# Kernel tuning notes

Measured on AMD Instinct MI355X. Metric: run time of the kernel, lower is better.

## Reference

```python
import jax, jax.numpy as jnp
import numpy as np

L_PAIRS = 2
K_NEG = 64
TEMP = 0.1
EPS = 1e-8  # torch F.cosine_similarity default eps


def _cos(a, b):
    # cosine similarity along last axis, torch-style eps clamping of norms
    na = jnp.maximum(jnp.linalg.norm(a, axis=-1), EPS)
    nb = jnp.maximum(jnp.linalg.norm(b, axis=-1), EPS)
    return jnp.sum(a * b, axis=-1) / (na * nb)


def setup_inputs() -> dict:
    D, N, d = 64, 4096, 512
    key = jax.random.key(0)
    k0, k1, k2, k3 = jax.random.split(key, 4)
    return {
        "I_embeddings": jax.random.normal(k0, (D, N, d), dtype=jnp.float32),
        "g0": jax.random.normal(k1, (d,), dtype=jnp.float32),
        "g1": jax.random.normal(k2, (d,), dtype=jnp.float32),
        "g2": jax.random.normal(k3, (d,), dtype=jnp.float32),
    }


def reference(I_embeddings, g0, g1, g2):
    D, N, d = I_embeddings.shape
    T = TEMP

    # per-embedding full sum: [D, d]
    sums = jnp.sum(I_embeddings, axis=1)

    # hard-negative sums: drop the top-K rows by L2 norm per embedding
    norms = jnp.linalg.norm(I_embeddings, axis=2)              # [D, N]
    _, topk_idx = jax.lax.top_k(norms, K_NEG)                  # [D, K]
    keep = jnp.ones((D, N), dtype=bool)
    keep = keep.at[jnp.arange(D)[:, None], topk_idx].set(False)
    sums_neg = jnp.sum(I_embeddings * keep[:, :, None], axis=1)  # [D, d]

    samples = jnp.concatenate([sums, sums_neg], axis=0)        # [2D, d]

    # positive pairs (i, i+L)
    P = D - L_PAIRS
    i_idx = jnp.arange(P)
    j_idx = i_idx + L_PAIRS

    # candidates per pair: arange(2D) with i and j removed (i < j)
    base = jnp.arange(2 * D - 2)                               # [2D-2]
    cand = base[None, :] + (base[None, :] >= i_idx[:, None]).astype(base.dtype)
    cand = cand + (cand >= j_idx[:, None]).astype(cand.dtype)  # [P, 2D-2]

    # random choice of K_NEG negatives per pair (deterministic key)
    key = jax.random.key(42)
    keys = jax.random.split(key, P)
    perm = jax.vmap(lambda k: jax.random.permutation(k, 2 * D - 2))(keys)[:, :K_NEG]
    sel = jnp.take_along_axis(cand, perm, axis=1)              # [P, K]
    negs = samples[sel]                                        # [P, K, d]

    pos_ij = _cos(g1, jax.lax.stop_gradient(g2)) / T           # scalar
    pos_ji = _cos(g2, jax.lax.stop_gradient(g1)) / T           # scalar

    s_i = sums[i_idx]                                          # [P, d]
    s_j = sums[j_idx]
    sim_i = _cos(s_i[:, None, :], negs) / T                    # [P, K]
    sim_j = _cos(s_j[:, None, :], negs) / T

    # -log( exp(pos) / (exp(pos) + sum exp(sim)) ) = logaddexp(pos, lse(sim)) - pos
    loss_i = jnp.logaddexp(pos_ij, jax.nn.logsumexp(sim_i, axis=1)) - pos_ij  # [P]
    loss_j = jnp.logaddexp(pos_ji, jax.nn.logsumexp(sim_j, axis=1)) - pos_ji

    return jnp.sum(loss_i + loss_j)
```

## Files before the change

kernel.cpp:

```cpp
#include <hip/hip_runtime.h>
#include <stdint.h>

#define D_EMB   64
#define N_ROWS  4096
#define DIM     512
#define KNEG    64
#define P_PAIRS 62
#define BPE     32
#define ROWS_PER_BLK (N_ROWS / BPE)
#define EPSN    1e-8f
#define INV_T   10.0f

__device__ __forceinline__ uint32_t rotl32(uint32_t v, uint32_t r) {
  return (v << r) | (v >> (32u - r));
}

__device__ __forceinline__ void threefry(uint32_t k0, uint32_t k1,
                                         uint32_t c0, uint32_t c1,
                                         uint32_t& o0, uint32_t& o1) {
  uint32_t ks0 = k0, ks1 = k1, ks2 = k0 ^ k1 ^ 0x1BD11BDAu;
  uint32_t x0 = c0 + ks0, x1 = c1 + ks1;
#define RG(a,b,c,d) \
  x0 += x1; x1 = rotl32(x1,a); x1 ^= x0; \
  x0 += x1; x1 = rotl32(x1,b); x1 ^= x0; \
  x0 += x1; x1 = rotl32(x1,c); x1 ^= x0; \
  x0 += x1; x1 = rotl32(x1,d); x1 ^= x0;
  RG(13,15,26,6)   x0 += ks1; x1 += ks2 + 1u;
  RG(17,29,16,24)  x0 += ks2; x1 += ks0 + 2u;
  RG(13,15,26,6)   x0 += ks0; x1 += ks1 + 3u;
  RG(17,29,16,24)  x0 += ks1; x1 += ks2 + 4u;
  RG(13,15,26,6)   x0 += ks2; x1 += ks0 + 5u;
#undef RG
  o0 = x0; o1 = x1;
}

__global__ __launch_bounds__(256, 8) void k_pass1(const float* __restrict__ I,
                                                  float* __restrict__ partial,
                                                  float* __restrict__ norms) {
  const int e = blockIdx.x / BPE, b = blockIdx.x % BPE;
  const int t = threadIdx.x, lane = t & 63, w = t >> 6;
  const float4* base = reinterpret_cast<const float4*>(I) + (size_t)e * N_ROWS * (DIM / 4);
  float acc[8] = {0.f,0.f,0.f,0.f,0.f,0.f,0.f,0.f};
  __shared__ float lds[4 * DIM];
  __shared__ float nlds[ROWS_PER_BLK];
  const int nbase = b * ROWS_PER_BLK;
  for (int i = 0; i < ROWS_PER_BLK / 4; ++i) {
    const int n = nbase + i * 4 + w;
    const float4* row = base + (size_t)n * (DIM / 4);
    float4 A = row[lane];
    float4 B = row[lane + 64];
    acc[0] += A.x; acc[1] += A.y; acc[2] += A.z; acc[3] += A.w;
    acc[4] += B.x; acc[5] += B.y; acc[6] += B.z; acc[7] += B.w;
    float sq = A.x*A.x + A.y*A.y + A.z*A.z + A.w*A.w
             + B.x*B.x + B.y*B.y + B.z*B.z + B.w*B.w;
#pragma unroll
    for (int off = 32; off; off >>= 1) sq += __shfl_xor(sq, off);
    if (lane == 0) nlds[i * 4 + w] = sqrtf(sq);
  }
  const int p0 = 4 * lane;
#pragma unroll
  for (int q = 0; q < 4; ++q) {
    lds[w * DIM + p0 + q]       = acc[q];
    lds[w * DIM + 256 + p0 + q] = acc[4 + q];
  }
  __syncthreads();
  float s0 = lds[t] + lds[DIM + t] + lds[2*DIM + t] + lds[3*DIM + t];
  float s1 = lds[256 + t] + lds[DIM + 256 + t] + lds[2*DIM + 256 + t] + lds[3*DIM + 256 + t];
  float* out = partial + (size_t)(e * BPE + b) * DIM;
  out[t] = s0;
  out[256 + t] = s1;
  if (t < ROWS_PER_BLK) norms[e * N_ROWS + nbase + t] = nlds[t];
}

__global__ __launch_bounds__(512) void k_embed(const float* __restrict__ I,
                                               const float* __restrict__ partial,
                                               const float* __restrict__ norms,
                                               const float* __restrict__ g1,
                                               const float* __restrict__ g2,
                                               float* __restrict__ samples,
                                               float* __restrict__ snorm,
                                               float* __restrict__ posp) {
  const int e = blockIdx.x;
  const int t = threadIdx.x, lane = t & 63, w = t >> 6;
  __shared__ float rA[8], rB[8], rC[8];

  if (e == D_EMB) {
    float x = g1[t], y = g2[t];
    float d = x * y, sa = x * x, sb = y * y;
#pragma unroll
    for (int off = 32; off; off >>= 1) {
      d  += __shfl_xor(d, off);
      sa += __shfl_xor(sa, off);
      sb += __shfl_xor(sb, off);
    }
    if (lane == 0) { rA[w] = d; rB[w] = sa; rC[w] = sb; }
    __syncthreads();
    if (t == 0) {
      float dt = 0.f, s1 = 0.f, s2 = 0.f;
      for (int q = 0; q < 8; ++q) { dt += rA[q]; s1 += rB[q]; s2 += rC[q]; }
      posp[0] = dt / (fmaxf(sqrtf(s1), EPSN) * fmaxf(sqrtf(s2), EPSN)) * INV_T;
    }
    return;
  }

  float v[8];
#pragma unroll
  for (int q = 0; q < 8; ++q) v[q] = norms[e * N_ROWS + q * DIM + t];
  float lmax = v[0]; int lidx = t;
#pragma unroll
  for (int q = 1; q < 8; ++q)
    if (v[q] > lmax) { lmax = v[q]; lidx = q * DIM + t; }

  __shared__ float wbv[8];
  __shared__ int   wbi[8];
  __shared__ int   topidx[KNEG];
  for (int k = 0; k < KNEG; ++k) {
    float bv = lmax; int bi = lidx;
#pragma unroll
    for (int off = 32; off; off >>= 1) {
      float ov = __shfl_xor(bv, off);
      int   oi = __shfl_xor(bi, off);
      if (ov > bv || (ov == bv && oi < bi)) { bv = ov; bi = oi; }
    }
    if (lane == 0) { wbv[w] = bv; wbi[w] = bi; }
    __syncthreads();
    float fv = wbv[0]; int fi = wbi[0];
#pragma unroll
    for (int q = 1; q < 8; ++q)
      if (wbv[q] > fv || (wbv[q] == fv && wbi[q] < fi)) { fv = wbv[q]; fi = wbi[q]; }
    if (t == (fi & (DIM - 1))) {
      v[fi >> 9] = -1e30f;
      lmax = v[0]; lidx = t;
#pragma unroll
      for (int q = 1; q < 8; ++q)
        if (v[q] > lmax) { lmax = v[q]; lidx = q * DIM + t; }
    }
    if (t == 0) topidx[k] = fi;
    __syncthreads();
  }

  float s = 0.f;
  for (int b2 = 0; b2 < BPE; ++b2)
    s += partial[(size_t)(e * BPE + b2) * DIM + t];

  const float* base = I + (size_t)e * N_ROWS * DIM;
  float a = 0.f;
#pragma unroll 4
  for (int k = 0; k < KNEG; ++k)
    a += base[(size_t)topidx[k] * DIM + t];
  float sn = s - a;

  float q1 = s * s, q2 = sn * sn;
#pragma unroll
  for (int off = 32; off; off >>= 1) {
    q1 += __shfl_xor(q1, off);
    q2 += __shfl_xor(q2, off);
  }
  if (lane == 0) { rA[w] = q1; rB[w] = q2; }
  __syncthreads();
  if (t == 0) {
    float n1 = 0.f, n2 = 0.f;
    for (int q = 0; q < 8; ++q) { n1 += rA[q]; n2 += rB[q]; }
    snorm[e]         = fmaxf(sqrtf(n1), EPSN);
    snorm[D_EMB + e] = fmaxf(sqrtf(n2), EPSN);
  }
  samples[(size_t)e * DIM + t]           = s;
  samples[(size_t)(D_EMB + e) * DIM + t] = sn;
}

__global__ __launch_bounds__(256) void k_pair(const float* __restrict__ samples,
                                              const float* __restrict__ snorm,
                                              const float* __restrict__ posp,
                                              float* __restrict__ pairloss) {
  const int p = blockIdx.x;
  const int t = threadIdx.x, lane = t & 63, w = t >> 6;
  __shared__ uint32_t bits[126];
  __shared__ uint32_t sk[2];
  __shared__ int      sel[KNEG];
  __shared__ float    simi[KNEG], simj[KNEG];

  if (t == 0) {
    uint32_t kh, kl, a, b;
    threefry(0u, 42u, 0u, (uint32_t)p, kh, kl);
    threefry(kh, kl, 0u, 1u, a, b);
    sk[0] = a; sk[1] = b;
  }
  __syncthreads();
  if (t < 126) {
    uint32_t a, b;
    threefry(sk[0], sk[1], 0u, (uint32_t)t, a, b);
    bits[t] = a ^ b;
  }
  __syncthreads();
  if (t < 126) {
    const uint32_t myb = bits[t];
    int rank = 0;
    for (int j = 0; j < 126; ++j) {
      const uint32_t bj = bits[j];
      rank += ((bj < myb) || (bj == myb && j < t)) ? 1 : 0;
    }
    if (rank < KNEG) {
      int vv = t + (t >= p ? 1 : 0);
      vv += (vv >= p + 2 ? 1 : 0);
      sel[rank] = vv;
    }
  }
  __syncthreads();

  const float4* S = reinterpret_cast<const float4*>(samples);
  const float4 siA = S[p * 128 + lane],       siB = S[p * 128 + 64 + lane];
  const float4 sjA = S[(p + 2) * 128 + lane], sjB = S[(p + 2) * 128 + 64 + lane];
  const float ni = snorm[p], nj = snorm[p + 2];
  for (int k = w; k < KNEG; k += 4) {
    const int r = sel[k];
    const float4 vA = S[r * 128 + lane], vB = S[r * 128 + 64 + lane];
    float di = siA.x*vA.x + siA.y*vA.y + siA.z*vA.z + siA.w*vA.w
             + siB.x*vB.x + siB.y*vB.y + siB.z*vB.z + siB.w*vB.w;
    float dj = sjA.x*vA.x + sjA.y*vA.y + sjA.z*vA.z + sjA.w*vA.w
             + sjB.x*vB.x + sjB.y*vB.y + sjB.z*vB.z + sjB.w*vB.w;
#pragma unroll
    for (int off = 32; off; off >>= 1) {
      di += __shfl_xor(di, off);
      dj += __shfl_xor(dj, off);
    }
    if (lane == 0) {
      const float nr = snorm[r];
      simi[k] = di / (ni * nr) * INV_T;
      simj[k] = dj / (nj * nr) * INV_T;
    }
  }
  __syncthreads();
  if (t < KNEG) {
    const float xi = simi[t], xj = simj[t];
    float mi = xi, mj = xj;
#pragma unroll
    for (int off = 32; off; off >>= 1) {
      mi = fmaxf(mi, __shfl_xor(mi, off));
      mj = fmaxf(mj, __shfl_xor(mj, off));
    }
    float ei = expf(xi - mi), ej = expf(xj - mj);
#pragma unroll
    for (int off = 32; off; off >>= 1) {
      ei += __shfl_xor(ei, off);
      ej += __shfl_xor(ej, off);
    }
    if (t == 0) {
      const float pos = posp[0];
      const float lsei = mi + logf(ei), lsej = mj + logf(ej);
      const float li = fmaxf(pos, lsei) + log1pf(expf(-fabsf(pos - lsei))) - pos;
      const float lj = fmaxf(pos, lsej) + log1pf(expf(-fabsf(pos - lsej))) - pos;
      pairloss[p] = li + lj;
    }
  }
}

__global__ __launch_bounds__(64) void k_final(const float* __restrict__ pairloss,
                                              float* __restrict__ out) {
  const int t = threadIdx.x;
  float v = (t < P_PAIRS) ? pairloss[t] : 0.f;
#pragma unroll
  for (int off = 32; off; off >>= 1) v += __shfl_xor(v, off);
  if (t == 0) out[0] = v;
}

extern "C" void kernel_launch(void* const* d_in, const int* in_sizes, int n_in,
                              void* d_out, int out_size, void* d_ws, size_t ws_size,
                              hipStream_t stream) {
  const float* I  = (const float*)d_in[0];
  const float* g1 = (const float*)d_in[2];
  const float* g2 = (const float*)d_in[3];
  float* out = (float*)d_out;

  float* ws = (float*)d_ws;
  float* norms    = ws;
  float* partial  = ws + 262144;
  float* samples  = partial + 1048576;
  float* snorm    = samples + 65536;
  float* posp     = snorm + 128;
  float* pairloss = posp + 4;

  k_pass1<<<D_EMB * BPE, 256, 0, stream>>>(I, partial, norms);
  k_embed<<<D_EMB + 1,   512, 0, stream>>>(I, partial, norms, g1, g2,
                                           samples, snorm, posp);
  k_pair <<<P_PAIRS,     256, 0, stream>>>(samples, snorm, posp, pairloss);
  k_final<<<1,            64, 0, stream>>>(pairloss, out);
}
```

Before: 207.3 us.

## Fuse all stages into one cooperative persistent kernel with grid syncs

Merges the four kernels into a single cooperative kernel that loops over row chunks and separates the phases with grid-wide syncs. A plain multi-kernel launch remains as a fallback. Per-embedding chunks drop from 32 to 16 and the embed stage shrinks from 512 to 256 threads. The aim is to remove launch gaps between the small tail kernels. In exchange, the streaming pass runs on a persistent grid limited by occupancy (4 blocks per CU), which may lower memory-level parallelism, and the host now queries device attributes and occupancy on every call.

Result: slower. 400.5 us (+93.2%).

```diff
diff --git a/kernel.cpp b/kernel.cpp
--- a/kernel.cpp
+++ b/kernel.cpp
@@ -1,13 +1,17 @@
 #include <hip/hip_runtime.h>
+#include <hip/hip_cooperative_groups.h>
 #include <stdint.h>
+
+namespace cg = cooperative_groups;
 
 #define D_EMB   64
 #define N_ROWS  4096
 #define DIM     512
 #define KNEG    64
 #define P_PAIRS 62
-#define BPE     32
-#define ROWS_PER_BLK (N_ROWS / BPE)
+#define BPE     16
+#define RPB     (N_ROWS / BPE)
+#define NCHUNK  (D_EMB * BPE)
 #define EPSN    1e-8f
 #define INV_T   10.0f
 
@@ -34,17 +38,26 @@
   o0 = x0; o1 = x1;
 }
 
-__global__ __launch_bounds__(256, 8) void k_pass1(const float* __restrict__ I,
-                                                  float* __restrict__ partial,
-                                                  float* __restrict__ norms) {
-  const int e = blockIdx.x / BPE, b = blockIdx.x % BPE;
-  const int t = threadIdx.x, lane = t & 63, w = t >> 6;
+struct Shm {
+  float    lds[4 * DIM];
+  float    nlds[RPB];
+  float    rA[4], rB[4], rC[4];
+  int      wbi[4];
+  int      topidx[KNEG];
+  uint32_t bits[126];
+  uint32_t sk[2];
+  int      sel[KNEG];
+  float    simi[KNEG], simj[KNEG];
+};
+
+__device__ void phase1(Shm& s, const float* __restrict__ I,
+                       float* __restrict__ partial, float* __restrict__ norms,
+                       int chunk, int t, int lane, int w) {
+  const int e = chunk >> 4, b = chunk & 15;
   const float4* base = reinterpret_cast<const float4*>(I) + (size_t)e * N_ROWS * (DIM / 4);
   float acc[8] = {0.f,0.f,0.f,0.f,0.f,0.f,0.f,0.f};
-  __shared__ float lds[4 * DIM];
-  __shared__ float nlds[ROWS_PER_BLK];
-  const int nbase = b * ROWS_PER_BLK;
-  for (int i = 0; i < ROWS_PER_BLK / 4; ++i) {
+  const int nbase = b * RPB;
+  for (int i = 0; i < RPB / 4; ++i) {
     const int n = nbase + i * 4 + w;
     const float4* row = base + (size_t)n * (DIM / 4);
     float4 A = row[lane];
@@ -55,65 +68,37 @@
              + B.x*B.x + B.y*B.y + B.z*B.z + B.w*B.w;
 #pragma unroll
     for (int off = 32; off; off >>= 1) sq += __shfl_xor(sq, off);
-    if (lane == 0) nlds[i * 4 + w] = sqrtf(sq);
+    if (lane == 0) s.nlds[i * 4 + w] = sqrtf(sq);
   }
   const int p0 = 4 * lane;
 #pragma unroll
   for (int q = 0; q < 4; ++q) {
-    lds[w * DIM + p0 + q]       = acc[q];
-    lds[w * DIM + 256 + p0 + q] = acc[4 + q];
-  }
-  __syncthreads();
-  float s0 = lds[t] + lds[DIM + t] + lds[2*DIM + t] + lds[3*DIM + t];
-  float s1 = lds[256 + t] + lds[DIM + 256 + t] + lds[2*DIM + 256 + t] + lds[3*DIM + 256 + t];
-  float* out = partial + (size_t)(e * BPE + b) * DIM;
-  out[t] = s0;
-  out[256 + t] = s1;
-  if (t < ROWS_PER_BLK) norms[e * N_ROWS + nbase + t] = nlds[t];
-}
-
-__global__ __launch_bounds__(512) void k_embed(const float* __restrict__ I,
-                                               const float* __restrict__ partial,
-                                               const float* __restrict__ norms,
-                                               const float* __restrict__ g1,
-                                               const float* __restrict__ g2,
-                                               float* __restrict__ samples,
-                                               float* __restrict__ snorm,
-                                               float* __restrict__ posp) {
-  const int e = blockIdx.x;
-  const int t = threadIdx.x, lane = t & 63, w = t >> 6;
-  __shared__ float rA[8], rB[8], rC[8];
-
-  if (e == D_EMB) {
-    float x = g1[t], y = g2[t];
-    float d = x * y, sa = x * x, sb = y * y;
-#pragma unroll
-    for (int off = 32; off; off >>= 1) {
-      d  += __shfl_xor(d, off);
-      sa += __shfl_xor(sa, off);
-      sb += __shfl_xor(sb, off);
-    }
-    if (lane == 0) { rA[w] = d; rB[w] = sa; rC[w] = sb; }
-    __syncthreads();
-    if (t == 0) {
-      float dt = 0.f, s1 = 0.f, s2 = 0.f;
-      for (int q = 0; q < 8; ++q) { dt += rA[q]; s1 += rB[q]; s2 += rC[q]; }
-      posp[0] = dt / (fmaxf(sqrtf(s1), EPSN) * fmaxf(sqrtf(s2), EPSN)) * INV_T;
-    }
-    return;
-  }
-
-  float v[8];
-#pragma unroll
-  for (int q = 0; q < 8; ++q) v[q] = norms[e * N_ROWS + q * DIM + t];
+    s.lds[w * DIM + p0 + q]       = acc[q];
+    s.lds[w * DIM + 256 + p0 + q] = acc[4 + q];
+  }
+  __syncthreads();
+  float s0 = s.lds[t] + s.lds[DIM + t] + s.lds[2*DIM + t] + s.lds[3*DIM + t];
+  float s1 = s.lds[256 + t] + s.lds[DIM + 256 + t] + s.lds[2*DIM + 256 + t] + s.lds[3*DIM + 256 + t];
+  float* po = partial + (size_t)chunk * DIM;
+  po[t] = s0;
+  po[256 + t] = s1;
+  norms[e * N_ROWS + nbase + t] = s.nlds[t];
+  __syncthreads();
+}
+
+__device__ void phase2(Shm& s, const float* __restrict__ I,
+                       const float* __restrict__ partial,
+                       const float* __restrict__ norms,
+                       float* __restrict__ samples, float* __restrict__ snorm,
+                       int e, int t, int lane, int w) {
+  float v[16];
+#pragma unroll
+  for (int q = 0; q < 16; ++q) v[q] = norms[e * N_ROWS + q * 256 + t];
   float lmax = v[0]; int lidx = t;
 #pragma unroll
-  for (int q = 1; q < 8; ++q)
-    if (v[q] > lmax) { lmax = v[q]; lidx = q * DIM + t; }
-
-  __shared__ float wbv[8];
-  __shared__ int   wbi[8];
-  __shared__ int   topidx[KNEG];
+  for (int q = 1; q < 16; ++q)
+    if (v[q] > lmax) { lmax = v[q]; lidx = q * 256 + t; }
+
   for (int k = 0; k < KNEG; ++k) {
     float bv = lmax; int bi = lidx;
 #pragma unroll
@@ -122,87 +107,108 @@
       int   oi = __shfl_xor(bi, off);
       if (ov > bv || (ov == bv && oi < bi)) { bv = ov; bi = oi; }
     }
-    if (lane == 0) { wbv[w] = bv; wbi[w] = bi; }
+    if (lane == 0) { s.rA[w] = bv; s.wbi[w] = bi; }
     __syncthreads();
-    float fv = wbv[0]; int fi = wbi[0];
-#pragma unroll
-    for (int q = 1; q < 8; ++q)
-      if (wbv[q] > fv || (wbv[q] == fv && wbi[q] < fi)) { fv = wbv[q]; fi = wbi[q]; }
-    if (t == (fi & (DIM - 1))) {
-      v[fi >> 9] = -1e30f;
+    float fv = s.rA[0]; int fi = s.wbi[0];
+#pragma unroll
+    for (int q = 1; q < 4; ++q)
+      if (s.rA[q] > fv || (s.rA[q] == fv && s.wbi[q] < fi)) { fv = s.rA[q]; fi = s.wbi[q]; }
+    if (t == (fi & 255)) {
+      v[fi >> 8] = -1e30f;
       lmax = v[0]; lidx = t;
 #pragma unroll
-      for (int q = 1; q < 8; ++q)
-        if (v[q] > lmax) { lmax = v[q]; lidx = q * DIM + t; }
-    }
-    if (t == 0) topidx[k] = fi;
+      for (int q = 1; q < 16; ++q)
+        if (v[q] > lmax) { lmax = v[q]; lidx = q * 256 + t; }
+    }
+    if (t == 0) s.topidx[k] = fi;
     __syncthreads();
   }
 
-  float s = 0.f;
-  for (int b2 = 0; b2 < BPE; ++b2)
-    s += partial[(size_t)(e * BPE + b2) * DIM + t];
-
+  float s0 = 0.f, s1 = 0.f;
+  for (int b2 = 0; b2 < BPE; ++b2) {
+    const float* pp = partial + (size_t)(e * BPE + b2) * DIM;
+    s0 += pp[t];
+    s1 += pp[256 + t];
+  }
   const float* base = I + (size_t)e * N_ROWS * DIM;
-  float a = 0.f;
+  float a0 = 0.f, a1 = 0.f;
 #pragma unroll 4
-  for (int k = 0; k < KNEG; ++k)
-    a += base[(size_t)topidx[k] * DIM + t];
-  float sn = s - a;
-
-  float q1 = s * s, q2 = sn * sn;
+  for (int k = 0; k < KNEG; ++k) {
+    const float* r = base + (size_t)s.topidx[k] * DIM;
+    a0 += r[t];
+    a1 += r[256 + t];
+  }
+  float sn0 = s0 - a0, sn1 = s1 - a1;
+
+  float q1 = s0 * s0 + s1 * s1, q2 = sn0 * sn0 + sn1 * sn1;
 #pragma unroll
   for (int off = 32; off; off >>= 1) {
     q1 += __shfl_xor(q1, off);
     q2 += __shfl_xor(q2, off);
   }
-  if (lane == 0) { rA[w] = q1; rB[w] = q2; }
+  if (lane == 0) { s.rA[w] = q1; s.rB[w] = q2; }
   __syncthreads();
   if (t == 0) {
-    float n1 = 0.f, n2 = 0.f;
-    for (int q = 0; q < 8; ++q) { n1 += rA[q]; n2 += rB[q]; }
+    float n1 = s.rA[0] + s.rA[1] + s.rA[2] + s.rA[3];
+    float n2 = s.rB[0] + s.rB[1] + s.rB[2] + s.rB[3];
     snorm[e]         = fmaxf(sqrtf(n1), EPSN);
     snorm[D_EMB + e] = fmaxf(sqrtf(n2), EPSN);
   }
-  samples[(size_t)e * DIM + t]           = s;
-  samples[(size_t)(D_EMB + e) * DIM + t] = sn;
-}
-
-__global__ __launch_bounds__(256) void k_pair(const float* __restrict__ samples,
-                                              const float* __restrict__ snorm,
-                                              const float* __restrict__ posp,
-                                              float* __restrict__ pairloss) {
-  const int p = blockIdx.x;
-  const int t = threadIdx.x, lane = t & 63, w = t >> 6;
-  __shared__ uint32_t bits[126];
-  __shared__ uint32_t sk[2];
-  __shared__ int      sel[KNEG];
-  __shared__ float    simi[KNEG], simj[KNEG];
-
+  samples[(size_t)e * DIM + t]                 = s0;
+  samples[(size_t)e * DIM + 256 + t]           = s1;
+  samples[(size_t)(D_EMB + e) * DIM + t]       = sn0;
+  samples[(size_t)(D_EMB + e) * DIM + 256 + t] = sn1;
+}
+
+__device__ void phase2pos(Shm& s, const float* __restrict__ g1,
+                          const float* __restrict__ g2,
+                          float* __restrict__ posp, int t, int lane, int w) {
+  float x0 = g1[t], x1 = g1[256 + t], y0 = g2[t], y1 = g2[256 + t];
+  float d = x0*y0 + x1*y1, sa = x0*x0 + x1*x1, sb = y0*y0 + y1*y1;
+#pragma unroll
+  for (int off = 32; off; off >>= 1) {
+    d  += __shfl_xor(d, off);
+    sa += __shfl_xor(sa, off);
+    sb += __shfl_xor(sb, off);
+  }
+  if (lane == 0) { s.rA[w] = d; s.rB[w] = sa; s.rC[w] = sb; }
+  __syncthreads();
+  if (t == 0) {
+    float dt = s.rA[0] + s.rA[1] + s.rA[2] + s.rA[3];
+    float s1 = s.rB[0] + s.rB[1] + s.rB[2] + s.rB[3];
+    float s2 = s.rC[0] + s.rC[1] + s.rC[2] + s.rC[3];
+    posp[0] = dt / (fmaxf(sqrtf(s1), EPSN) * fmaxf(sqrtf(s2), EPSN)) * INV_T;
+  }
+}
+
+__device__ void phase3(Shm& s, const float* __restrict__ samples,
+                       const float* __restrict__ snorm,
+                       const float* __restrict__ posp,
+                       float* __restrict__ pairloss, int p, int t, int lane, int w) {
   if (t == 0) {
     uint32_t kh, kl, a, b;
     threefry(0u, 42u, 0u, (uint32_t)p, kh, kl);
     threefry(kh, kl, 0u, 1u, a, b);
-    sk[0] = a; sk[1] = b;
+    s.sk[0] = a; s.sk[1] = b;
   }
   __syncthreads();
   if (t < 126) {
     uint32_t a, b;
-    threefry(sk[0], sk[1], 0u, (uint32_t)t, a, b);
-    bits[t] = a ^ b;
+    threefry(s.sk[0], s.sk[1], 0u, (uint32_t)t, a, b);
+    s.bits[t] = a ^ b;
   }
   __syncthreads();
   if (t < 126) {
-    const uint32_t myb = bits[t];
+    const uint32_t myb = s.bits[t];
     int rank = 0;
     for (int j = 0; j < 126; ++j) {
-      const uint32_t bj = bits[j];
+      const uint32_t bj = s.bits[j];
       rank += ((bj < myb) || (bj == myb && j < t)) ? 1 : 0;
     }
     if (rank < KNEG) {
       int vv = t + (t >= p ? 1 : 0);
       vv += (vv >= p + 2 ? 1 : 0);
-      sel[rank] = vv;
+      s.sel[rank] = vv;
     }
   }
   __syncthreads();
@@ -212,7 +218,7 @@
   const float4 sjA = S[(p + 2) * 128 + lane], sjB = S[(p + 2) * 128 + 64 + lane];
   const float ni = snorm[p], nj = snorm[p + 2];
   for (int k = w; k < KNEG; k += 4) {
-    const int r = sel[k];
+    const int r = s.sel[k];
     const float4 vA = S[r * 128 + lane], vB = S[r * 128 + 64 + lane];
     float di = siA.x*vA.x + siA.y*vA.y + siA.z*vA.z + siA.w*vA.w
              + siB.x*vB.x + siB.y*vB.y + siB.z*vB.z + siB.w*vB.w;
@@ -225,13 +231,13 @@
     }
     if (lane == 0) {
       const float nr = snorm[r];
-      simi[k] = di / (ni * nr) * INV_T;
-      simj[k] = dj / (nj * nr) * INV_T;
+      s.simi[k] = di / (ni * nr) * INV_T;
+      s.simj[k] = dj / (nj * nr) * INV_T;
     }
   }
   __syncthreads();
   if (t < KNEG) {
-    const float xi = simi[t], xj = simj[t];
+    const float xi = s.simi[t], xj = s.simj[t];
     float mi = xi, mj = xj;
 #pragma unroll
     for (int off = 32; off; off >>= 1) {
@@ -254,13 +260,83 @@
   }
 }
 
-__global__ __launch_bounds__(64) void k_final(const float* __restrict__ pairloss,
-                                              float* __restrict__ out) {
+__device__ void phase4(const float* __restrict__ pairloss, float* __restrict__ out, int t) {
+  if (t < 64) {
+    float vv = (t < P_PAIRS) ? pairloss[t] : 0.f;
+#pragma unroll
+    for (int off = 32; off; off >>= 1) vv += __shfl_xor(vv, off);
+    if (t == 0) out[0] = vv;
+  }
+}
+
+__global__ __launch_bounds__(256, 4) void k_all(const float* __restrict__ I,
+                                                const float* __restrict__ g1,
+                                                const float* __restrict__ g2,
+                                                float* __restrict__ partial,
+                                                float* __restrict__ norms,
+                                                float* __restrict__ samples,
+                                                float* __restrict__ snorm,
+                                                float* __restrict__ posp,
+                                                float* __restrict__ pairloss,
+                                                float* __restrict__ out) {
+  cg::grid_group grid = cg::this_grid();
+  const int t = threadIdx.x, lane = t & 63, w = t >> 6;
+  __shared__ Shm s;
+
+  for (int c = blockIdx.x; c < NCHUNK; c += gridDim.x)
+    phase1(s, I, partial, norms, c, t, lane, w);
+  grid.sync();
+
+  if (blockIdx.x < D_EMB)
+    phase2(s, I, partial, norms, samples, snorm, blockIdx.x, t, lane, w);
+  else if (blockIdx.x == D_EMB)
+    phase2pos(s, g1, g2, posp, t, lane, w);
+  grid.sync();
+
+  if (blockIdx.x < P_PAIRS)
+    phase3(s, samples, snorm, posp, pairloss, blockIdx.x, t, lane, w);
+  grid.sync();
+
+  if (blockIdx.x == 0)
+    phase4(pairloss, out, t);
+}
+
+__global__ __launch_bounds__(256) void k_p1(const float* __restrict__ I,
+                                            float* __restrict__ partial,
+                                            float* __restrict__ norms) {
+  __shared__ Shm s;
   const int t = threadIdx.x;
-  float v = (t < P_PAIRS) ? pairloss[t] : 0.f;
-#pragma unroll
-  for (int off = 32; off; off >>= 1) v += __shfl_xor(v, off);
-  if (t == 0) out[0] = v;
+  phase1(s, I, partial, norms, blockIdx.x, t, t & 63, t >> 6);
+}
+
+__global__ __launch_bounds__(256) void k_p2(const float* __restrict__ I,
+                                            const float* __restrict__ partial,
+                                            const float* __restrict__ norms,
+                                            const float* __restrict__ g1,
+                                            const float* __restrict__ g2,
+                                            float* __restrict__ samples,
+                                            float* __restrict__ snorm,
+                                            float* __restrict__ posp) {
+  __shared__ Shm s;
+  const int t = threadIdx.x;
+  if (blockIdx.x < D_EMB)
+    phase2(s, I, partial, norms, samples, snorm, blockIdx.x, t, t & 63, t >> 6);
+  else
+    phase2pos(s, g1, g2, posp, t, t & 63, t >> 6);
+}
+
+__global__ __launch_bounds__(256) void k_p3(const float* __restrict__ samples,
+                                            const float* __restrict__ snorm,
+                                            const float* __restrict__ posp,
+                                            float* __restrict__ pairloss) {
+  __shared__ Shm s;
+  const int t = threadIdx.x;
+  phase3(s, samples, snorm, posp, pairloss, blockIdx.x, t, t & 63, t >> 6);
+}
+
+__global__ __launch_bounds__(64) void k_p4(const float* __restrict__ pairloss,
+                                           float* __restrict__ out) {
+  phase4(pairloss, out, threadIdx.x);
 }
 
 extern "C" void kernel_launch(void* const* d_in, const int* in_sizes, int n_in,
@@ -274,14 +350,33 @@
   float* ws = (float*)d_ws;
   float* norms    = ws;
   float* partial  = ws + 262144;
-  float* samples  = partial + 1048576;
+  float* samples  = partial + 524288;
   float* snorm    = samples + 65536;
   float* posp     = snorm + 128;
   float* pairloss = posp + 4;
 
-  k_pass1<<<D_EMB * BPE, 256, 0, stream>>>(I, partial, norms);
-  k_embed<<<D_EMB + 1,   512, 0, stream>>>(I, partial, norms, g1, g2,
-                                           samples, snorm, posp);
-  k_pair <<<P_PAIRS,     256, 0, stream>>>(samples, snorm, posp, pairloss);
-  k_final<<<1,            64, 0, stream>>>(pairloss, out);
-}
+  int dev = 0, coop = 0, ncu = 0, occ = 0;
+  bool ok = (hipGetDevice(&dev) == hipSuccess);
+  if (ok) hipDeviceGetAttribute(&coop, hipDeviceAttributeCooperativeLaunch, dev);
+  if (ok) hipDeviceGetAttribute(&ncu, hipDeviceAttributeMultiprocessorCount, dev);
+  if (ok && coop && ncu > 0) {
+    if (hipOccupancyMaxActiveBlocksPerMultiprocessor(&occ, (const void*)k_all,
+                                                     256, 0) != hipSuccess)
+      occ = 0;
+  }
+  long maxb = (long)occ * (long)ncu;
+  if (ok && coop && maxb >= D_EMB + 2) {
+    int nblk = (int)(maxb < NCHUNK ? maxb : NCHUNK);
+    void* args[] = { (void*)&I, (void*)&g1, (void*)&g2,
+                     (void*)&partial, (void*)&norms, (void*)&samples,
+                     (void*)&snorm, (void*)&posp, (void*)&pairloss, (void*)&out };
+    if (hipLaunchCooperativeKernel((const void*)k_all, dim3(nblk), dim3(256),
+                                   args, 0, stream) == hipSuccess)
+      return;
+  }
+
+  k_p1<<<NCHUNK,    256, 0, stream>>>(I, partial, norms);
+  k_p2<<<D_EMB + 1, 256, 0, stream>>>(I, partial, norms, g1, g2, samples, snorm, posp);
+  k_p3<<<P_PAIRS,   256, 0, stream>>>(samples, snorm, posp, pairloss);
+  k_p4<<<1,          64, 0, stream>>>(pairloss, out);
+}
```
